# Optimization experiments

Measured on AMD Instinct MI355X. Metric: run time of the kernel, lower is better.

The kernel has to match this reference:

```python
import jax, jax.numpy as jnp
import numpy as np

B, A = 64, 32            # graphs, atoms per graph
N, E = B * A, B * A * A  # nodes, fully-connected edges (incl. self-loops)
H, LAT = 512, 256        # hidden_dim, latent_dim
L = 4                    # num CSP layers
NF = 10                  # sinusoid frequencies -> dis_dim = 2*NF*3 = 60
MAXA = 100
DIS = 2 * NF * 3
EIN = 2 * H + 9 + DIS    # edge_mlp input width = 1093


def _lin(k, fan_in, shape):
    return jax.random.normal(k, shape, jnp.float32) * (1.0 / np.sqrt(fan_in))


def setup_inputs() -> dict:
    key = jax.random.key(0)
    ks = jax.random.split(key, 20)
    t = jax.random.normal(ks[0], (B, LAT), jnp.float32)
    atom_types = jax.random.randint(ks[1], (N,), 1, MAXA + 1, dtype=jnp.int32)
    frac_coords = jax.random.uniform(ks[2], (N, 3), jnp.float32)
    lattices = jax.random.normal(ks[3], (B, 3, 3), jnp.float32)
    node2graph = jnp.repeat(jnp.arange(B, dtype=jnp.int32), A)
    # fc edges per graph, row-major like dense_to_sparse(block_diag(ones))
    base = (np.arange(B, dtype=np.int64) * A)[:, None]
    ii = np.repeat(np.arange(A), A)
    jj = np.tile(np.arange(A), A)
    src = (base + ii[None, :]).reshape(-1)
    dst = (base + jj[None, :]).reshape(-1)
    edge_index = jnp.asarray(np.stack([src, dst]), dtype=jnp.int32)
    params = dict(
        emb_table=jax.random.normal(ks[4], (MAXA, H), jnp.float32),
        W_latent=_lin(ks[5], H + LAT, (H + LAT, H)), b_latent=jnp.zeros((H,), jnp.float32),
        edge_W1=_lin(ks[6], EIN, (L, EIN, H)), edge_b1=jnp.zeros((L, H), jnp.float32),
        edge_W2=_lin(ks[7], H, (L, H, H)), edge_b2=jnp.zeros((L, H), jnp.float32),
        node_W1=_lin(ks[8], 2 * H, (L, 2 * H, H)), node_b1=jnp.zeros((L, H), jnp.float32),
        node_W2=_lin(ks[9], H, (L, H, H)), node_b2=jnp.zeros((L, H), jnp.float32),
        coord_W=_lin(ks[10], H, (H, 3)),
        lattice_W=_lin(ks[11], H, (H, 9)),
    )
    return dict(t=t, frac_coords=frac_coords, lattices=lattices, **params,
                atom_types=atom_types, node2graph=node2graph, edge_index=edge_index)


def reference(t, frac_coords, lattices, emb_table, W_latent, b_latent,
              edge_W1, edge_b1, edge_W2, edge_b2,
              node_W1, node_b1, node_W2, node_b2,
              coord_W, lattice_W, atom_types, node2graph, edge_index):
    silu = jax.nn.silu
    src, dst = edge_index[0], edge_index[1]
    edge2graph = node2graph[src]
    # gen_edges (fc): frac_diff per edge
    frac_diff = (frac_coords[dst] - frac_coords[src]) % 1.0            # [E,3]
    # SinusoidsEmbedding (same for every layer)
    freqs = 2.0 * jnp.pi * jnp.arange(NF, dtype=jnp.float32)
    fd = (frac_diff[:, :, None] * freqs).reshape(-1, 3 * NF)
    fd_emb = jnp.concatenate([jnp.sin(fd), jnp.cos(fd)], axis=-1)      # [E,60]
    # lattice inner products (ip=True), broadcast to edges
    lat_ip = jnp.einsum('bij,bkj->bik', lattices, lattices).reshape(-1, 9)
    lat_e = lat_ip[edge2graph]                                          # [E,9]
    # node embedding + time conditioning
    nf = emb_table[atom_types - 1]                                      # [N,H]
    nf = jnp.concatenate([nf, t[node2graph]], axis=1) @ W_latent + b_latent
    ones_e = jnp.ones((src.shape[0], 1), nf.dtype)
    for i in range(L):
        hi, hj = nf[src], nf[dst]
        ein = jnp.concatenate([hi, hj, lat_e, fd_emb], axis=1)          # [E,1093]
        ef = silu(silu(ein @ edge_W1[i] + edge_b1[i]) @ edge_W2[i] + edge_b2[i])
        agg = jax.ops.segment_sum(ef, src, num_segments=N)
        deg = jax.ops.segment_sum(ones_e, src, num_segments=N)
        agg = agg / jnp.maximum(deg, 1.0)                               # scatter-mean
        nin = jnp.concatenate([nf, agg], axis=1)                        # [N,2H]
        nf = nf + silu(silu(nin @ node_W1[i] + node_b1[i]) @ node_W2[i] + node_b2[i])
    coord_out = nf @ coord_W                                            # [N,3]
    gf = jax.ops.segment_sum(nf, node2graph, num_segments=B) / A        # graph mean
    lattice_out = (gf @ lattice_W).reshape(-1, 3, 3)
    lattice_out = jnp.einsum('bij,bjk->bik', lattice_out, lattices)     # ip=True
    return (lattice_out, coord_out)
```

## Files before the change

### kernel.cpp

```cpp
#include <hip/hip_runtime.h>
#include <math.h>


typedef short bf16x8 __attribute__((ext_vector_type(8)));
typedef float f32x4 __attribute__((ext_vector_type(4)));

__device__ __forceinline__ float silu_f(float x) {
    float e = __builtin_amdgcn_exp2f(x * -1.44269504088896f);
    return x * __builtin_amdgcn_rcpf(1.0f + e);
}
__device__ __forceinline__ unsigned short f2bf(float x) {
    unsigned int u = __float_as_uint(x);
    u += 0x7fffu + ((u >> 16) & 1u);
    return (unsigned short)(u >> 16);
}
__device__ __forceinline__ unsigned int cvt_pk_bf16(float lo, float hi) {
    unsigned int r;
    asm("v_cvt_pk_bf16_f32 %0, %1, %2" : "=v"(r) : "v"(lo), "v"(hi));
    return r;
}

#define NF_OFF    0
#define UAGG_OFF  (2048*512)
#define VTD_OFF   (2*2048*512)
#define H1_OFF    (VTD_OFF + 64*16384)
#define WBF_OFF   (H1_OFF + 524288)
#define SZ_INITT (512*768)
#define SZ_UVT   (1024*512)
#define SZ_W1DT  (512*64)
#define SZ_W2T   (512*512)
#define SZ_NW1T  (512*1024)
#define SZ_NW2T  (512*512)
#define SZ_LAYER (SZ_UVT+SZ_W1DT+SZ_W2T+SZ_NW1T+SZ_NW2T)
#define WBF_FLOATS ((SZ_INITT + 4*SZ_LAYER + 1)/2)
#define FDP_OFF   (WBF_OFF + WBF_FLOATS)

__global__ __launch_bounds__(256) void k_prep(
    const float* __restrict__ Wl, const float* __restrict__ eW1,
    const float* __restrict__ eW2, const float* __restrict__ nW1,
    const float* __restrict__ nW2, unsigned short* __restrict__ wbf)
{
    __shared__ float tile[32][33];
    int bid = blockIdx.x;
    const float* src; int K; unsigned short* dst; int t;
    if (bid < 384) { src = Wl; K = 768; dst = wbf; t = bid; }
    else {
        int b = bid - 384; int l = b / 1568; int j = b - l * 1568;
        const float* e1 = eW1 + (size_t)l * 1093 * 512;
        unsigned short* base = wbf + SZ_INITT + (size_t)l * SZ_LAYER;
        if (j < 256)      { src = e1;                       K = 512;  dst = base;                                   t = j; }
        else if (j < 512) { src = e1 + 512*512;             K = 512;  dst = base + 512*512;                         t = j-256; }
        else if (j < 544) { src = e1 + 1033*512;            K = 60;   dst = base + SZ_UVT;                          t = j-512; }
        else if (j < 800) { src = eW2 + (size_t)l*512*512;  K = 512;  dst = base + SZ_UVT+SZ_W1DT;                  t = j-544; }
        else if (j <1312) { src = nW1 + (size_t)l*1024*512; K = 1024; dst = base + SZ_UVT+SZ_W1DT+SZ_W2T;           t = j-800; }
        else              { src = nW2 + (size_t)l*512*512;  K = 512;  dst = base + SZ_UVT+SZ_W1DT+SZ_W2T+SZ_NW1T;   t = j-1312; }
    }
    int tr = t >> 4, tc = t & 15;
    int k0 = tr * 32, nn0 = tc * 32;
    {
        int r8 = threadIdx.x >> 5, cc = threadIdx.x & 31;
        #pragma unroll
        for (int rr = 0; rr < 4; ++rr) {
            int row = rr*8 + r8;
            int k = k0 + row;
            tile[row][cc] = (k < K) ? src[(size_t)k*512 + nn0 + cc] : 0.f;
        }
    }
    __syncthreads();
    int nt_loc = threadIdx.x >> 7;
    int l = (threadIdx.x >> 1) & 63;
    int jh = threadIdx.x & 1;
    int lj = l & 15, lh = l >> 4;
    float v0 = tile[lh*8 + jh*4 + 0][nt_loc*16 + lj];
    float v1 = tile[lh*8 + jh*4 + 1][nt_loc*16 + lj];
    float v2 = tile[lh*8 + jh*4 + 2][nt_loc*16 + lj];
    float v3 = tile[lh*8 + jh*4 + 3][nt_loc*16 + lj];
    uint2 pk = { cvt_pk_bf16(v0, v1), cvt_pk_bf16(v2, v3) };
    *(uint2*)&dst[((size_t)(tr*32 + tc*2 + nt_loc)*64 + l)*8 + jh*4] = pk;
}

__global__ __launch_bounds__(64) void k_fd(const float* __restrict__ frac,
                                           unsigned short* __restrict__ fdP)
{
    int bid = blockIdx.x;
    int n0 = bid * 2, g = n0 >> 5;
    int l = threadIdx.x, lj = l & 15, lh = l >> 4;
    float di[2][2][3];
    #pragma unroll
    for (int h = 0; h < 2; ++h)
        #pragma unroll
        for (int dd = 0; dd < 2; ++dd) {
            int dstn = g*32 + dd*16 + lj;
            #pragma unroll
            for (int comp = 0; comp < 3; ++comp) {
                float d = frac[dstn*3 + comp] - frac[(n0+h)*3 + comp];
                d -= floorf(d);
                di[h][dd][comp] = d;
            }
        }
    #pragma unroll
    for (int kt = 0; kt < 2; ++kt)
        #pragma unroll
        for (int mt = 0; mt < 4; ++mt) {
            int h = mt >> 1, dd = mt & 1;
            unsigned int w[4];
            #pragma unroll
            for (int p = 0; p < 4; ++p) {
                float vv[2];
                #pragma unroll
                for (int e = 0; e < 2; ++e) {
                    int k = kt*32 + lh*8 + p*2 + e;
                    float val = 0.f;
                    if (k < 60) {
                        int isCos = k >= 30;
                        int dq = k - (isCos ? 30 : 0);
                        int comp = dq >= 20 ? 2 : (dq >= 10 ? 1 : 0);
                        int f = dq - comp*10;
                        float u = di[h][dd][comp] * (float)f;
                        u -= floorf(u);
                        val = isCos ? __builtin_amdgcn_cosf(u) : __builtin_amdgcn_sinf(u);
                    }
                    vv[e] = val;
                }
                w[p] = cvt_pk_bf16(vv[0], vv[1]);
            }
            uint4 pk = { w[0], w[1], w[2], w[3] };
            *(uint4*)&fdP[(((size_t)bid*8 + kt*4 + mt)*64 + l)*8] = pk;
        }
}

__global__ __launch_bounds__(256) void k_init(
    const float* __restrict__ tvec, const float* __restrict__ emb,
    const unsigned short* __restrict__ WT, const float* __restrict__ bl,
    const int* __restrict__ atom_types, float* __restrict__ nf)
{
    __shared__ __align__(16) unsigned short cat_s[16*768];
    int n0 = (blockIdx.x >> 1) * 16, half = blockIdx.x & 1, tid = threadIdx.x;
    for (int idx = tid; idx < 16*192; idx += 256) {
        int m = idx / 192, q = idx - m * 192;
        int k4 = q * 4, n = n0 + m;
        float4 v;
        if (k4 < 512) v = *(const float4*)&emb[(size_t)(atom_types[n]-1)*512 + k4];
        else          v = *(const float4*)&tvec[(size_t)(n>>5)*256 + (k4-512)];
        uint2 pk = { cvt_pk_bf16(v.x, v.y), cvt_pk_bf16(v.z, v.w) };
        *(uint2*)&cat_s[m*768 + (k4 ^ ((m&7)<<3))] = pk;
    }
    __syncthreads();
    int w = tid >> 6, l = tid & 63, lj = l & 15, lh = l >> 4;
    f32x4 acc[4];
    #pragma unroll
    for (int nt = 0; nt < 4; ++nt) acc[nt] = (f32x4){0.f,0.f,0.f,0.f};
    for (int kt = 0; kt < 24; ++kt) {
        int k = kt*32 + lh*8;
        bf16x8 a = *(const bf16x8*)&cat_s[lj*768 + (k ^ ((lj&7)<<3))];
        #pragma unroll
        for (int nt = 0; nt < 4; ++nt) {
            bf16x8 b = *(const bf16x8*)&WT[(((size_t)kt*32 + half*16 + w*4 + nt)*64 + l)*8];
            acc[nt] = __builtin_amdgcn_mfma_f32_16x16x32_bf16(a, b, acc[nt], 0, 0, 0);
        }
    }
    #pragma unroll
    for (int nt = 0; nt < 4; ++nt) {
        int c = half*256 + w*64 + nt*16 + lj;
        float bv = bl[c];
        #pragma unroll
        for (int r = 0; r < 4; ++r)
            nf[(size_t)(n0 + lh*4 + r)*512 + c] = acc[nt][r] + bv;
    }
}

__global__ __launch_bounds__(256) void k_uv(
    const float* __restrict__ nf, const unsigned short* __restrict__ WT,
    const float* __restrict__ lat, const float* __restrict__ W1c,
    const float* __restrict__ b1, float* __restrict__ Up,
    float* __restrict__ VTD)
{
    __shared__ __align__(16) unsigned short a_s[16*512];
    int ng = blockIdx.x >> 2, half = (blockIdx.x >> 1) & 1, ch = blockIdx.x & 1;
    int n0 = ng * 16, g = n0 >> 5, tid = threadIdx.x;
    for (int idx = tid; idx < 16*128; idx += 256) {
        int m = idx >> 7, q = idx & 127;
        int k4 = q * 4;
        float4 v = *(const float4*)&nf[(size_t)(n0+m)*512 + k4];
        uint2 pk = { cvt_pk_bf16(v.x, v.y), cvt_pk_bf16(v.z, v.w) };
        *(uint2*)&a_s[m*512 + (k4 ^ ((m&7)<<3))] = pk;
    }
    __syncthreads();
    int w = tid >> 6, l = tid & 63, lj = l & 15, lh = l >> 4;
    const unsigned short* Wh = WT + (size_t)half*512*512;
    f32x4 acc[4];
    #pragma unroll
    for (int nt = 0; nt < 4; ++nt) acc[nt] = (f32x4){0.f,0.f,0.f,0.f};
    for (int kt = 0; kt < 16; ++kt) {
        int k = kt*32 + lh*8;
        bf16x8 a = *(const bf16x8*)&a_s[lj*512 + (k ^ ((lj&7)<<3))];
        #pragma unroll
        for (int nt = 0; nt < 4; ++nt) {
            bf16x8 b = *(const bf16x8*)&Wh[(((size_t)kt*32 + ch*16 + w*4 + nt)*64 + l)*8];
            acc[nt] = __builtin_amdgcn_mfma_f32_16x16x32_bf16(a, b, acc[nt], 0, 0, 0);
        }
    }
    if (half == 0) {
        float L[9], lip[9];
        #pragma unroll
        for (int i = 0; i < 9; ++i) L[i] = lat[g*9 + i];
        #pragma unroll
        for (int i = 0; i < 3; ++i)
            #pragma unroll
            for (int kk = 0; kk < 3; ++kk)
                lip[i*3+kk] = L[i*3]*L[kk*3] + L[i*3+1]*L[kk*3+1] + L[i*3+2]*L[kk*3+2];
        #pragma unroll
        for (int nt = 0; nt < 4; ++nt) {
            int c = ch*256 + w*64 + nt*16 + lj;
            float p3 = b1[c];
            #pragma unroll
            for (int t9 = 0; t9 < 9; ++t9) p3 += lip[t9] * W1c[t9*512 + c];
            #pragma unroll
            for (int r = 0; r < 4; ++r)
                Up[(size_t)(n0 + lh*4 + r)*512 + c] = acc[nt][r] + p3;
        }
    } else {
        int dd = (n0 & 31) >> 4;
        #pragma unroll
        for (int nt = 0; nt < 4; ++nt) {
            int ct = ch*16 + w*4 + nt;
            #pragma unroll
            for (int rr = 0; rr < 4; ++rr)
                VTD[(size_t)g*16384 + ct*512 + dd*256 + (lh*4+rr)*16 + lj] = acc[nt][rr];
        }
    }
}

__global__ __launch_bounds__(512) void k_edge(
    const float* __restrict__ Up, const float* __restrict__ VTD,
    const unsigned short* __restrict__ fdP,
    const unsigned short* __restrict__ W1dT,
    const unsigned short* __restrict__ W2T, const float* __restrict__ b2,
    float* __restrict__ agg)
{
    __shared__ __align__(16) unsigned short ef1_s[64*512];
    int n0 = blockIdx.x * 2, g = n0 >> 5, tid = threadIdx.x;
    int wid = tid >> 6, l = tid & 63, lj = l & 15, lh = l >> 4;

    {
        bf16x8 fdf[2][4];
        #pragma unroll
        for (int kt = 0; kt < 2; ++kt)
            #pragma unroll
            for (int mt = 0; mt < 4; ++mt)
                fdf[kt][mt] = *(const bf16x8*)&fdP[(((size_t)blockIdx.x*8 + kt*4 + mt)*64 + l)*8];

        #pragma unroll
        for (int q = 0; q < 4; ++q) {
            int ct = wid*4 + q;
            f32x4 a1[4];
            #pragma unroll
            for (int mt = 0; mt < 4; ++mt)
                a1[mt] = *(const f32x4*)&VTD[(size_t)g*16384 + ct*512 + (mt&1)*256 + lj*16 + lh*4];
            #pragma unroll
            for (int kt = 0; kt < 2; ++kt) {
                bf16x8 wf = *(const bf16x8*)&W1dT[(((size_t)kt*32 + ct)*64 + l)*8];
                #pragma unroll
                for (int mt = 0; mt < 4; ++mt)
                    a1[mt] = __builtin_amdgcn_mfma_f32_16x16x32_bf16(wf, fdf[kt][mt], a1[mt], 0, 0, 0);
            }
            int c0 = wid*64 + q*16 + lh*4;
            float4 bs0 = *(const float4*)&Up[(size_t)n0*512 + c0];
            float4 bs1 = *(const float4*)&Up[(size_t)(n0+1)*512 + c0];
            #pragma unroll
            for (int mt = 0; mt < 4; ++mt) {
                float4 bb = (mt >> 1) ? bs1 : bs0;
                int m = mt*16 + lj;
                float x0 = silu_f(a1[mt][0] + bb.x);
                float x1 = silu_f(a1[mt][1] + bb.y);
                float x2 = silu_f(a1[mt][2] + bb.z);
                float x3 = silu_f(a1[mt][3] + bb.w);
                uint2 pk = { cvt_pk_bf16(x0, x1), cvt_pk_bf16(x2, x3) };
                *(uint2*)&ef1_s[m*512 + (c0 ^ ((m&7)<<3))] = pk;
            }
        }
    }
    __syncthreads();

    f32x4 acc2[4][4];
    #pragma unroll
    for (int mt = 0; mt < 4; ++mt)
        #pragma unroll
        for (int nt = 0; nt < 4; ++nt) acc2[mt][nt] = (f32x4){0.f,0.f,0.f,0.f};

    for (int kt = 0; kt < 16; ++kt) {
        int k = kt*32 + lh*8;
        bf16x8 af[4];
        #pragma unroll
        for (int mt = 0; mt < 4; ++mt) {
            int m = mt*16 + lj;
            af[mt] = *(const bf16x8*)&ef1_s[m*512 + (k ^ ((m&7)<<3))];
        }
        __builtin_amdgcn_s_setprio(1);
        #pragma unroll
        for (int nt = 0; nt < 4; ++nt) {
            bf16x8 bfr = *(const bf16x8*)&W2T[(((size_t)kt*32 + wid*4 + nt)*64 + l)*8];
            #pragma unroll
            for (int mt = 0; mt < 4; ++mt)
                acc2[mt][nt] = __builtin_amdgcn_mfma_f32_16x16x32_bf16(af[mt], bfr, acc2[mt][nt], 0, 0, 0);
        }
        __builtin_amdgcn_s_setprio(0);
    }

    #pragma unroll
    for (int nt = 0; nt < 4; ++nt) {
        int cc = wid*64 + nt*16 + lj;
        float bv = b2[cc];
        float s0 = 0.f, s1 = 0.f;
        #pragma unroll
        for (int mt = 0; mt < 4; ++mt)
            #pragma unroll
            for (int r = 0; r < 4; ++r) {
                float x = silu_f(acc2[mt][nt][r] + bv);
                if (mt < 2) s0 += x; else s1 += x;
            }
        s0 += __shfl_xor(s0, 16); s0 += __shfl_xor(s0, 32);
        s1 += __shfl_xor(s1, 16); s1 += __shfl_xor(s1, 32);
        if (lh == 0) {
            agg[(size_t)n0*512 + cc]     = s0 * (1.0f/32.0f);
            agg[(size_t)(n0+1)*512 + cc] = s1 * (1.0f/32.0f);
        }
    }
}

__global__ __launch_bounds__(256) void k_node1(
    const float* __restrict__ nf, const float* __restrict__ agg,
    const unsigned short* __restrict__ W1T, const float* __restrict__ b1,
    unsigned short* __restrict__ h1g)
{
    __shared__ __align__(16) unsigned short nin_s[16*1024];
    int ng = blockIdx.x >> 2, cq = blockIdx.x & 3;
    int n0 = ng * 16, tid = threadIdx.x;
    for (int idx = tid; idx < 16*256; idx += 256) {
        int m = idx >> 8, q = idx & 255;
        int k4 = q * 4;
        float4 v = (k4 < 512) ? *(const float4*)&nf[(size_t)(n0+m)*512 + k4]
                              : *(const float4*)&agg[(size_t)(n0+m)*512 + (k4-512)];
        uint2 pk = { cvt_pk_bf16(v.x, v.y), cvt_pk_bf16(v.z, v.w) };
        *(uint2*)&nin_s[m*1024 + (k4 ^ ((m&7)<<3))] = pk;
    }
    __syncthreads();
    int w = tid >> 6, l = tid & 63, lj = l & 15, lh = l >> 4;
    f32x4 acc[2];
    acc[0] = (f32x4){0.f,0.f,0.f,0.f};
    acc[1] = (f32x4){0.f,0.f,0.f,0.f};
    for (int kt = 0; kt < 32; ++kt) {
        int k = kt*32 + lh*8;
        bf16x8 a = *(const bf16x8*)&nin_s[lj*1024 + (k ^ ((lj&7)<<3))];
        #pragma unroll
        for (int nt = 0; nt < 2; ++nt) {
            bf16x8 b = *(const bf16x8*)&W1T[(((size_t)kt*32 + cq*8 + w*2 + nt)*64 + l)*8];
            acc[nt] = __builtin_amdgcn_mfma_f32_16x16x32_bf16(a, b, acc[nt], 0, 0, 0);
        }
    }
    #pragma unroll
    for (int nt = 0; nt < 2; ++nt) {
        int c = cq*128 + w*32 + nt*16 + lj;
        float bv = b1[c];
        #pragma unroll
        for (int r = 0; r < 4; ++r)
            h1g[(size_t)(n0 + lh*4 + r)*512 + c] = f2bf(silu_f(acc[nt][r] + bv));
    }
}

__global__ __launch_bounds__(256) void k_node2(
    float* __restrict__ nf, const unsigned short* __restrict__ h1g,
    const unsigned short* __restrict__ W2T, const float* __restrict__ b2)
{
    __shared__ __align__(16) unsigned short h1_s[16*512];
    int ng = blockIdx.x >> 2, cq = blockIdx.x & 3;
    int n0 = ng * 16, tid = threadIdx.x;
    for (int idx = tid; idx < 16*64; idx += 256) {
        int m = idx >> 6, k8 = (idx & 63) * 8;
        bf16x8 v = *(const bf16x8*)&h1g[(size_t)(n0+m)*512 + k8];
        *(bf16x8*)&h1_s[m*512 + (k8 ^ ((m&7)<<3))] = v;
    }
    __syncthreads();
    int w = tid >> 6, l = tid & 63, lj = l & 15, lh = l >> 4;
    f32x4 acc[2];
    acc[0] = (f32x4){0.f,0.f,0.f,0.f};
    acc[1] = (f32x4){0.f,0.f,0.f,0.f};
    for (int kt = 0; kt < 16; ++kt) {
        int k = kt*32 + lh*8;
        bf16x8 a = *(const bf16x8*)&h1_s[lj*512 + (k ^ ((lj&7)<<3))];
        #pragma unroll
        for (int nt = 0; nt < 2; ++nt) {
            bf16x8 b = *(const bf16x8*)&W2T[(((size_t)kt*32 + cq*8 + w*2 + nt)*64 + l)*8];
            acc[nt] = __builtin_amdgcn_mfma_f32_16x16x32_bf16(a, b, acc[nt], 0, 0, 0);
        }
    }
    #pragma unroll
    for (int nt = 0; nt < 2; ++nt) {
        int c = cq*128 + w*32 + nt*16 + lj;
        float bv = b2[c];
        #pragma unroll
        for (int r = 0; r < 4; ++r) {
            size_t o = (size_t)(n0 + lh*4 + r)*512 + c;
            nf[o] = nf[o] + silu_f(acc[nt][r] + bv);
        }
    }
}

__global__ __launch_bounds__(256) void k_coord(const float* __restrict__ nf,
                                               const float* __restrict__ cW,
                                               float* __restrict__ out) {
    int b = blockIdx.x, t = threadIdx.x;
    int nl = t >> 3, s = t & 7;
    int n = b*32 + nl;
    const float* row = nf + (size_t)n*512 + s*64;
    float p0 = 0.f, p1 = 0.f, p2 = 0.f;
    #pragma unroll
    for (int k4 = 0; k4 < 64; k4 += 4) {
        float4 v = *(const float4*)&row[k4];
        int kg = s*64 + k4;
        p0 += v.x*cW[(kg+0)*3+0] + v.y*cW[(kg+1)*3+0] + v.z*cW[(kg+2)*3+0] + v.w*cW[(kg+3)*3+0];
        p1 += v.x*cW[(kg+0)*3+1] + v.y*cW[(kg+1)*3+1] + v.z*cW[(kg+2)*3+1] + v.w*cW[(kg+3)*3+1];
        p2 += v.x*cW[(kg+0)*3+2] + v.y*cW[(kg+1)*3+2] + v.z*cW[(kg+2)*3+2] + v.w*cW[(kg+3)*3+2];
    }
    p0 += __shfl_xor(p0, 1); p0 += __shfl_xor(p0, 2); p0 += __shfl_xor(p0, 4);
    p1 += __shfl_xor(p1, 1); p1 += __shfl_xor(p1, 2); p1 += __shfl_xor(p1, 4);
    p2 += __shfl_xor(p2, 1); p2 += __shfl_xor(p2, 2); p2 += __shfl_xor(p2, 4);
    if (s == 0) {
        out[576 + n*3 + 0] = p0;
        out[576 + n*3 + 1] = p1;
        out[576 + n*3 + 2] = p2;
    }
}

__global__ __launch_bounds__(256) void k_graph(const float* __restrict__ nf,
                                               const float* __restrict__ lW,
                                               const float* __restrict__ lat,
                                               float* __restrict__ out) {
    __shared__ float gf[512];
    __shared__ float lo9[9];
    int b = blockIdx.x, tid = threadIdx.x;
    float s0 = 0.f, s1 = 0.f;
    for (int r = 0; r < 32; ++r) {
        s0 += nf[(b * 32 + r) * 512 + tid];
        s1 += nf[(b * 32 + r) * 512 + tid + 256];
    }
    gf[tid]       = s0 * (1.f / 32.f);
    gf[tid + 256] = s1 * (1.f / 32.f);
    __syncthreads();
    if (tid < 9) {
        float s = 0.f;
        for (int k = 0; k < 512; ++k) s += gf[k] * lW[k * 9 + tid];
        lo9[tid] = s;
    }
    __syncthreads();
    if (tid < 9) {
        int i = tid / 3, kk = tid - (tid / 3) * 3;
        float s = lo9[i*3+0] * lat[b*9 + 0*3 + kk]
                + lo9[i*3+1] * lat[b*9 + 1*3 + kk]
                + lo9[i*3+2] * lat[b*9 + 2*3 + kk];
        out[b * 9 + tid] = s;
    }
}

extern "C" void kernel_launch(void* const* d_in, const int* in_sizes, int n_in,
                              void* d_out, int out_size, void* d_ws, size_t ws_size,
                              hipStream_t stream)
{
    const float* t    = (const float*)d_in[0];
    const float* frac = (const float*)d_in[1];
    const float* lat  = (const float*)d_in[2];
    const float* emb  = (const float*)d_in[3];
    const float* Wl   = (const float*)d_in[4];
    const float* bl   = (const float*)d_in[5];
    const float* eW1  = (const float*)d_in[6];
    const float* eb1  = (const float*)d_in[7];
    const float* eW2  = (const float*)d_in[8];
    const float* eb2  = (const float*)d_in[9];
    const float* nW1  = (const float*)d_in[10];
    const float* nb1  = (const float*)d_in[11];
    const float* nW2  = (const float*)d_in[12];
    const float* nb2  = (const float*)d_in[13];
    const float* cW   = (const float*)d_in[14];
    const float* lW   = (const float*)d_in[15];
    const int* atom_types = (const int*)d_in[16];

    float* out  = (float*)d_out;
    float* wsf  = (float*)d_ws;
    float* nf   = wsf + NF_OFF;
    float* Uagg = wsf + UAGG_OFF;
    float* VTD  = wsf + VTD_OFF;
    unsigned short* h1g = (unsigned short*)(wsf + H1_OFF);
    unsigned short* wbf = (unsigned short*)(wsf + WBF_OFF);
    unsigned short* fdP = (unsigned short*)(wsf + FDP_OFF);

    k_prep<<<384 + 4*1568, 256, 0, stream>>>(Wl, eW1, eW2, nW1, nW2, wbf);
    k_fd<<<1024, 64, 0, stream>>>(frac, fdP);
    k_init<<<256, 256, 0, stream>>>(t, emb, wbf, bl, atom_types, nf);
    for (int l = 0; l < 4; ++l) {
        const unsigned short* base = wbf + SZ_INITT + (size_t)l * SZ_LAYER;
        const unsigned short* w1dT = base + SZ_UVT;
        const unsigned short* w2T  = w1dT + SZ_W1DT;
        const unsigned short* nw1T = w2T + SZ_W2T;
        const unsigned short* nw2T = nw1T + SZ_NW1T;
        k_uv<<<512, 256, 0, stream>>>(nf, base, lat,
                                      eW1 + (size_t)l*1093*512 + 1024*512,
                                      eb1 + l*512, Uagg, VTD);
        k_edge<<<1024, 512, 0, stream>>>(Uagg, VTD, fdP, w1dT, w2T,
                                         eb2 + l*512, Uagg);
        k_node1<<<512, 256, 0, stream>>>(nf, Uagg, nw1T, nb1 + l*512, h1g);
        k_node2<<<512, 256, 0, stream>>>(nf, h1g, nw2T, nb2 + l*512);
    }
    k_coord<<<64, 256, 0, stream>>>(nf, cW, out);
    k_graph<<<64, 256, 0, stream>>>(nf, lW, lat, out);
}
```

Measured before the change: 386.8 us.

## Store activations in MFMA-packed bf16 layout and register-prefetch GEMM operands

Producers (k_init, k_edge, k_node1, k_node2) now also write node features, aggregates and hidden activations as bf16 directly in the MFMA A-fragment order. Consumers can then load operand fragments straight from global memory instead of converting fp32 to bf16 through swizzled LDS staging with a barrier. The node GEMM loops and the k_edge second GEMM add register double-buffering of the A/B fragments for the next k-step. The cost is extra scattered 2-byte stores in the epilogues and higher register pressure from the prefetch buffers. Agg is also now stored in bf16 only, which lowers its precision slightly.

Measured after the change: 355.4 us. 1.09x faster.

```diff
diff --git a/kernel.cpp b/kernel.cpp
--- a/kernel.cpp
+++ b/kernel.cpp
@@ -19,12 +19,17 @@
     asm("v_cvt_pk_bf16_f32 %0, %1, %2" : "=v"(r) : "v"(lo), "v"(hi));
     return r;
 }
+__device__ __forceinline__ size_t apack_idx(int ng, int m, int c) {
+    return ((size_t)(ng*16 + (c >> 5))*64 + (m + 16*((c >> 3) & 3)))*8 + (c & 7);
+}
 
 #define NF_OFF    0
-#define UAGG_OFF  (2048*512)
+#define UP_OFF    (2048*512)
 #define VTD_OFF   (2*2048*512)
-#define H1_OFF    (VTD_OFF + 64*16384)
-#define WBF_OFF   (H1_OFF + 524288)
+#define NFP_OFF   (VTD_OFF + 1048576)
+#define H1P_OFF   (NFP_OFF + 524288)
+#define AGGP_OFF  (H1P_OFF + 524288)
+#define WBF_OFF   (AGGP_OFF + 524288)
 #define SZ_INITT (512*768)
 #define SZ_UVT   (1024*512)
 #define SZ_W1DT  (512*64)
@@ -132,10 +137,12 @@
 __global__ __launch_bounds__(256) void k_init(
     const float* __restrict__ tvec, const float* __restrict__ emb,
     const unsigned short* __restrict__ WT, const float* __restrict__ bl,
-    const int* __restrict__ atom_types, float* __restrict__ nf)
+    const int* __restrict__ atom_types, float* __restrict__ nf,
+    unsigned short* __restrict__ nfP)
 {
     __shared__ __align__(16) unsigned short cat_s[16*768];
-    int n0 = (blockIdx.x >> 1) * 16, half = blockIdx.x & 1, tid = threadIdx.x;
+    int ng = blockIdx.x >> 1, half = blockIdx.x & 1;
+    int n0 = ng * 16, tid = threadIdx.x;
     for (int idx = tid; idx < 16*192; idx += 256) {
         int m = idx / 192, q = idx - m * 192;
         int k4 = q * 4, n = n0 + m;
@@ -164,41 +171,46 @@
         int c = half*256 + w*64 + nt*16 + lj;
         float bv = bl[c];
         #pragma unroll
-        for (int r = 0; r < 4; ++r)
-            nf[(size_t)(n0 + lh*4 + r)*512 + c] = acc[nt][r] + bv;
+        for (int r = 0; r < 4; ++r) {
+            int m = lh*4 + r;
+            float v = acc[nt][r] + bv;
+            nf[(size_t)(n0 + m)*512 + c] = v;
+            nfP[apack_idx(ng, m, c)] = f2bf(v);
+        }
     }
 }
 
 __global__ __launch_bounds__(256) void k_uv(
-    const float* __restrict__ nf, const unsigned short* __restrict__ WT,
+    const unsigned short* __restrict__ nfP, const unsigned short* __restrict__ WT,
     const float* __restrict__ lat, const float* __restrict__ W1c,
     const float* __restrict__ b1, float* __restrict__ Up,
     float* __restrict__ VTD)
 {
-    __shared__ __align__(16) unsigned short a_s[16*512];
     int ng = blockIdx.x >> 2, half = (blockIdx.x >> 1) & 1, ch = blockIdx.x & 1;
     int n0 = ng * 16, g = n0 >> 5, tid = threadIdx.x;
-    for (int idx = tid; idx < 16*128; idx += 256) {
-        int m = idx >> 7, q = idx & 127;
-        int k4 = q * 4;
-        float4 v = *(const float4*)&nf[(size_t)(n0+m)*512 + k4];
-        uint2 pk = { cvt_pk_bf16(v.x, v.y), cvt_pk_bf16(v.z, v.w) };
-        *(uint2*)&a_s[m*512 + (k4 ^ ((m&7)<<3))] = pk;
-    }
-    __syncthreads();
     int w = tid >> 6, l = tid & 63, lj = l & 15, lh = l >> 4;
     const unsigned short* Wh = WT + (size_t)half*512*512;
     f32x4 acc[4];
     #pragma unroll
     for (int nt = 0; nt < 4; ++nt) acc[nt] = (f32x4){0.f,0.f,0.f,0.f};
+    bf16x8 acur, anxt, bcur[4], bnxt[4];
+    acur = *(const bf16x8*)&nfP[((size_t)(ng*16 + 0)*64 + l)*8];
+    #pragma unroll
+    for (int nt = 0; nt < 4; ++nt)
+        bcur[nt] = *(const bf16x8*)&Wh[(((size_t)0*32 + ch*16 + w*4 + nt)*64 + l)*8];
     for (int kt = 0; kt < 16; ++kt) {
-        int k = kt*32 + lh*8;
-        bf16x8 a = *(const bf16x8*)&a_s[lj*512 + (k ^ ((lj&7)<<3))];
-        #pragma unroll
-        for (int nt = 0; nt < 4; ++nt) {
-            bf16x8 b = *(const bf16x8*)&Wh[(((size_t)kt*32 + ch*16 + w*4 + nt)*64 + l)*8];
-            acc[nt] = __builtin_amdgcn_mfma_f32_16x16x32_bf16(a, b, acc[nt], 0, 0, 0);
-        }
+        if (kt < 15) {
+            anxt = *(const bf16x8*)&nfP[((size_t)(ng*16 + kt + 1)*64 + l)*8];
+            #pragma unroll
+            for (int nt = 0; nt < 4; ++nt)
+                bnxt[nt] = *(const bf16x8*)&Wh[(((size_t)(kt+1)*32 + ch*16 + w*4 + nt)*64 + l)*8];
+        }
+        #pragma unroll
+        for (int nt = 0; nt < 4; ++nt)
+            acc[nt] = __builtin_amdgcn_mfma_f32_16x16x32_bf16(acur, bcur[nt], acc[nt], 0, 0, 0);
+        acur = anxt;
+        #pragma unroll
+        for (int nt = 0; nt < 4; ++nt) bcur[nt] = bnxt[nt];
     }
     if (half == 0) {
         float L[9], lip[9];
@@ -236,7 +248,7 @@
     const unsigned short* __restrict__ fdP,
     const unsigned short* __restrict__ W1dT,
     const unsigned short* __restrict__ W2T, const float* __restrict__ b2,
-    float* __restrict__ agg)
+    unsigned short* __restrict__ aggP)
 {
     __shared__ __align__(16) unsigned short ef1_s[64*512];
     int n0 = blockIdx.x * 2, g = n0 >> 5, tid = threadIdx.x;
@@ -288,6 +300,11 @@
         #pragma unroll
         for (int nt = 0; nt < 4; ++nt) acc2[mt][nt] = (f32x4){0.f,0.f,0.f,0.f};
 
+    bf16x8 bcur[4], bnxt[4];
+    #pragma unroll
+    for (int nt = 0; nt < 4; ++nt)
+        bcur[nt] = *(const bf16x8*)&W2T[(((size_t)0*32 + wid*4 + nt)*64 + l)*8];
+
     for (int kt = 0; kt < 16; ++kt) {
         int k = kt*32 + lh*8;
         bf16x8 af[4];
@@ -296,17 +313,24 @@
             int m = mt*16 + lj;
             af[mt] = *(const bf16x8*)&ef1_s[m*512 + (k ^ ((m&7)<<3))];
         }
+        if (kt < 15) {
+            #pragma unroll
+            for (int nt = 0; nt < 4; ++nt)
+                bnxt[nt] = *(const bf16x8*)&W2T[(((size_t)(kt+1)*32 + wid*4 + nt)*64 + l)*8];
+        }
         __builtin_amdgcn_s_setprio(1);
         #pragma unroll
         for (int nt = 0; nt < 4; ++nt) {
-            bf16x8 bfr = *(const bf16x8*)&W2T[(((size_t)kt*32 + wid*4 + nt)*64 + l)*8];
             #pragma unroll
             for (int mt = 0; mt < 4; ++mt)
-                acc2[mt][nt] = __builtin_amdgcn_mfma_f32_16x16x32_bf16(af[mt], bfr, acc2[mt][nt], 0, 0, 0);
+                acc2[mt][nt] = __builtin_amdgcn_mfma_f32_16x16x32_bf16(af[mt], bcur[nt], acc2[mt][nt], 0, 0, 0);
         }
         __builtin_amdgcn_s_setprio(0);
-    }
-
+        #pragma unroll
+        for (int nt = 0; nt < 4; ++nt) bcur[nt] = bnxt[nt];
+    }
+
+    int ngg = n0 >> 4, m0 = n0 & 15;
     #pragma unroll
     for (int nt = 0; nt < 4; ++nt) {
         int cc = wid*64 + nt*16 + lj;
@@ -322,77 +346,85 @@
         s0 += __shfl_xor(s0, 16); s0 += __shfl_xor(s0, 32);
         s1 += __shfl_xor(s1, 16); s1 += __shfl_xor(s1, 32);
         if (lh == 0) {
-            agg[(size_t)n0*512 + cc]     = s0 * (1.0f/32.0f);
-            agg[(size_t)(n0+1)*512 + cc] = s1 * (1.0f/32.0f);
+            aggP[apack_idx(ngg, m0,     cc)] = f2bf(s0 * (1.0f/32.0f));
+            aggP[apack_idx(ngg, m0 + 1, cc)] = f2bf(s1 * (1.0f/32.0f));
         }
     }
 }
 
 __global__ __launch_bounds__(256) void k_node1(
-    const float* __restrict__ nf, const float* __restrict__ agg,
+    const unsigned short* __restrict__ nfP, const unsigned short* __restrict__ aggP,
     const unsigned short* __restrict__ W1T, const float* __restrict__ b1,
-    unsigned short* __restrict__ h1g)
-{
-    __shared__ __align__(16) unsigned short nin_s[16*1024];
-    int ng = blockIdx.x >> 2, cq = blockIdx.x & 3;
-    int n0 = ng * 16, tid = threadIdx.x;
-    for (int idx = tid; idx < 16*256; idx += 256) {
-        int m = idx >> 8, q = idx & 255;
-        int k4 = q * 4;
-        float4 v = (k4 < 512) ? *(const float4*)&nf[(size_t)(n0+m)*512 + k4]
-                              : *(const float4*)&agg[(size_t)(n0+m)*512 + (k4-512)];
-        uint2 pk = { cvt_pk_bf16(v.x, v.y), cvt_pk_bf16(v.z, v.w) };
-        *(uint2*)&nin_s[m*1024 + (k4 ^ ((m&7)<<3))] = pk;
-    }
-    __syncthreads();
+    unsigned short* __restrict__ h1P)
+{
+    int ng = blockIdx.x >> 2, cq = blockIdx.x & 3, tid = threadIdx.x;
     int w = tid >> 6, l = tid & 63, lj = l & 15, lh = l >> 4;
     f32x4 acc[2];
     acc[0] = (f32x4){0.f,0.f,0.f,0.f};
     acc[1] = (f32x4){0.f,0.f,0.f,0.f};
+    bf16x8 acur, anxt, bcur[2], bnxt[2];
+    acur = *(const bf16x8*)&nfP[((size_t)(ng*16 + 0)*64 + l)*8];
+    #pragma unroll
+    for (int nt = 0; nt < 2; ++nt)
+        bcur[nt] = *(const bf16x8*)&W1T[(((size_t)0*32 + cq*8 + w*2 + nt)*64 + l)*8];
     for (int kt = 0; kt < 32; ++kt) {
-        int k = kt*32 + lh*8;
-        bf16x8 a = *(const bf16x8*)&nin_s[lj*1024 + (k ^ ((lj&7)<<3))];
-        #pragma unroll
-        for (int nt = 0; nt < 2; ++nt) {
-            bf16x8 b = *(const bf16x8*)&W1T[(((size_t)kt*32 + cq*8 + w*2 + nt)*64 + l)*8];
-            acc[nt] = __builtin_amdgcn_mfma_f32_16x16x32_bf16(a, b, acc[nt], 0, 0, 0);
-        }
+        if (kt < 31) {
+            int kn = kt + 1;
+            anxt = (kn < 16)
+                ? *(const bf16x8*)&nfP[((size_t)(ng*16 + kn)*64 + l)*8]
+                : *(const bf16x8*)&aggP[((size_t)(ng*16 + kn - 16)*64 + l)*8];
+            #pragma unroll
+            for (int nt = 0; nt < 2; ++nt)
+                bnxt[nt] = *(const bf16x8*)&W1T[(((size_t)kn*32 + cq*8 + w*2 + nt)*64 + l)*8];
+        }
+        #pragma unroll
+        for (int nt = 0; nt < 2; ++nt)
+            acc[nt] = __builtin_amdgcn_mfma_f32_16x16x32_bf16(acur, bcur[nt], acc[nt], 0, 0, 0);
+        acur = anxt;
+        #pragma unroll
+        for (int nt = 0; nt < 2; ++nt) bcur[nt] = bnxt[nt];
     }
     #pragma unroll
     for (int nt = 0; nt < 2; ++nt) {
         int c = cq*128 + w*32 + nt*16 + lj;
         float bv = b1[c];
         #pragma unroll
-        for (int r = 0; r < 4; ++r)
-            h1g[(size_t)(n0 + lh*4 + r)*512 + c] = f2bf(silu_f(acc[nt][r] + bv));
+        for (int r = 0; r < 4; ++r) {
+            int m = lh*4 + r;
+            h1P[apack_idx(ng, m, c)] = f2bf(silu_f(acc[nt][r] + bv));
+        }
     }
 }
 
 __global__ __launch_bounds__(256) void k_node2(
-    float* __restrict__ nf, const unsigned short* __restrict__ h1g,
-    const unsigned short* __restrict__ W2T, const float* __restrict__ b2)
-{
-    __shared__ __align__(16) unsigned short h1_s[16*512];
-    int ng = blockIdx.x >> 2, cq = blockIdx.x & 3;
-    int n0 = ng * 16, tid = threadIdx.x;
-    for (int idx = tid; idx < 16*64; idx += 256) {
-        int m = idx >> 6, k8 = (idx & 63) * 8;
-        bf16x8 v = *(const bf16x8*)&h1g[(size_t)(n0+m)*512 + k8];
-        *(bf16x8*)&h1_s[m*512 + (k8 ^ ((m&7)<<3))] = v;
-    }
-    __syncthreads();
+    float* __restrict__ nf, const unsigned short* __restrict__ h1P,
+    const unsigned short* __restrict__ W2T, const float* __restrict__ b2,
+    unsigned short* __restrict__ nfP)
+{
+    int ng = blockIdx.x >> 2, cq = blockIdx.x & 3, tid = threadIdx.x;
+    int n0 = ng * 16;
     int w = tid >> 6, l = tid & 63, lj = l & 15, lh = l >> 4;
     f32x4 acc[2];
     acc[0] = (f32x4){0.f,0.f,0.f,0.f};
     acc[1] = (f32x4){0.f,0.f,0.f,0.f};
+    bf16x8 acur, anxt, bcur[2], bnxt[2];
+    acur = *(const bf16x8*)&h1P[((size_t)(ng*16 + 0)*64 + l)*8];
+    #pragma unroll
+    for (int nt = 0; nt < 2; ++nt)
+        bcur[nt] = *(const bf16x8*)&W2T[(((size_t)0*32 + cq*8 + w*2 + nt)*64 + l)*8];
     for (int kt = 0; kt < 16; ++kt) {
-        int k = kt*32 + lh*8;
-        bf16x8 a = *(const bf16x8*)&h1_s[lj*512 + (k ^ ((lj&7)<<3))];
-        #pragma unroll
-        for (int nt = 0; nt < 2; ++nt) {
-            bf16x8 b = *(const bf16x8*)&W2T[(((size_t)kt*32 + cq*8 + w*2 + nt)*64 + l)*8];
-            acc[nt] = __builtin_amdgcn_mfma_f32_16x16x32_bf16(a, b, acc[nt], 0, 0, 0);
-        }
+        if (kt < 15) {
+            anxt = *(const bf16x8*)&h1P[((size_t)(ng*16 + kt + 1)*64 + l)*8];
+            #pragma unroll
+            for (int nt = 0; nt < 2; ++nt)
+                bnxt[nt] = *(const bf16x8*)&W2T[(((size_t)(kt+1)*32 + cq*8 + w*2 + nt)*64 + l)*8];
+        }
+        #pragma unroll
+        for (int nt = 0; nt < 2; ++nt)
+            acc[nt] = __builtin_amdgcn_mfma_f32_16x16x32_bf16(acur, bcur[nt], acc[nt], 0, 0, 0);
+        acur = anxt;
+        #pragma unroll
+        for (int nt = 0; nt < 2; ++nt) bcur[nt] = bnxt[nt];
     }
     #pragma unroll
     for (int nt = 0; nt < 2; ++nt) {
@@ -400,8 +432,11 @@
         float bv = b2[c];
         #pragma unroll
         for (int r = 0; r < 4; ++r) {
-            size_t o = (size_t)(n0 + lh*4 + r)*512 + c;
-            nf[o] = nf[o] + silu_f(acc[nt][r] + bv);
+            int m = lh*4 + r;
+            size_t o = (size_t)(n0 + m)*512 + c;
+            float v = nf[o] + silu_f(acc[nt][r] + bv);
+            nf[o] = v;
+            nfP[apack_idx(ng, m, c)] = f2bf(v);
         }
     }
 }
@@ -487,28 +522,30 @@
     float* out  = (float*)d_out;
     float* wsf  = (float*)d_ws;
     float* nf   = wsf + NF_OFF;
-    float* Uagg = wsf + UAGG_OFF;
+    float* Up   = wsf + UP_OFF;
     float* VTD  = wsf + VTD_OFF;
-    unsigned short* h1g = (unsigned short*)(wsf + H1_OFF);
-    unsigned short* wbf = (unsigned short*)(wsf + WBF_OFF);
-    unsigned short* fdP = (unsigned short*)(wsf + FDP_OFF);
+    unsigned short* nfP  = (unsigned short*)(wsf + NFP_OFF);
+    unsigned short* h1P  = (unsigned short*)(wsf + H1P_OFF);
+    unsigned short* aggP = (unsigned short*)(wsf + AGGP_OFF);
+    unsigned short* wbf  = (unsigned short*)(wsf + WBF_OFF);
+    unsigned short* fdP  = (unsigned short*)(wsf + FDP_OFF);
 
     k_prep<<<384 + 4*1568, 256, 0, stream>>>(Wl, eW1, eW2, nW1, nW2, wbf);
     k_fd<<<1024, 64, 0, stream>>>(frac, fdP);
-    k_init<<<256, 256, 0, stream>>>(t, emb, wbf, bl, atom_types, nf);
+    k_init<<<256, 256, 0, stream>>>(t, emb, wbf, bl, atom_types, nf, nfP);
     for (int l = 0; l < 4; ++l) {
         const unsigned short* base = wbf + SZ_INITT + (size_t)l * SZ_LAYER;
         const unsigned short* w1dT = base + SZ_UVT;
         const unsigned short* w2T  = w1dT + SZ_W1DT;
         const unsigned short* nw1T = w2T + SZ_W2T;
         const unsigned short* nw2T = nw1T + SZ_NW1T;
-        k_uv<<<512, 256, 0, stream>>>(nf, base, lat,
+        k_uv<<<512, 256, 0, stream>>>(nfP, base, lat,
                                       eW1 + (size_t)l*1093*512 + 1024*512,
-                                      eb1 + l*512, Uagg, VTD);
-        k_edge<<<1024, 512, 0, stream>>>(Uagg, VTD, fdP, w1dT, w2T,
-                                         eb2 + l*512, Uagg);
-        k_node1<<<512, 256, 0, stream>>>(nf, Uagg, nw1T, nb1 + l*512, h1g);
-        k_node2<<<512, 256, 0, stream>>>(nf, h1g, nw2T, nb2 + l*512);
+                                      eb1 + l*512, Up, VTD);
+        k_edge<<<1024, 512, 0, stream>>>(Up, VTD, fdP, w1dT, w2T,
+                                         eb2 + l*512, aggP);
+        k_node1<<<512, 256, 0, stream>>>(nfP, aggP, nw1T, nb1 + l*512, h1P);
+        k_node2<<<512, 256, 0, stream>>>(nf, h1P, nw2T, nb2 + l*512, nfP);
     }
     k_coord<<<64, 256, 0, stream>>>(nf, cW, out);
     k_graph<<<64, 256, 0, stream>>>(nf, lW, lat, out);
```
